# Performance work log

Measured on AMD Instinct MI355X. Metric: run time of the kernel, lower is better.

## Reference

```python
import jax, jax.numpy as jnp
import numpy as np

STEEPNESS = 10.0
EPS = 1e-12

def _l2norm(x):
    return x / jnp.sqrt(jnp.sum(x * x, axis=-1, keepdims=True) + EPS)

def setup_inputs() -> dict:
    key = jax.random.key(0)
    k1, k2, k3 = jax.random.split(key, 3)
    B, D, C = 65536, 512, 1024
    return {
        "query": jax.random.normal(k1, (B, D), dtype=jnp.float32),
        "key_mem": jax.random.normal(k2, (C, D), dtype=jnp.float32),
        "val_mem": jax.random.normal(k3, (C, C), dtype=jnp.float32),
    }

def reference(query, key_mem, val_mem):
    # F.normalize(query_vectors, dim=-1)
    q = _l2norm(query)                      # (B, D)
    # cosine_similarity_multi(q, key_mem, rep='real'):
    # F.linear(F.normalize(a), F.normalize(b)) -> (B, C)
    k = _l2norm(key_mem)                    # (C, D)
    sim = jnp.einsum('bd,cd->bc', q, k)     # (B, C)
    # softabs sharpening: sigmoid(s*(x-0.5)) + sigmoid(s*(-x-0.5))
    s = STEEPNESS
    sharp = jax.nn.sigmoid(s * sim - 0.5 * s) + jax.nn.sigmoid(-s * sim - 0.5 * s)
    # normalize_weightings
    w = sharp / jnp.sum(sharp, axis=1, keepdims=True)
    # weighted value readout
    out = jnp.matmul(w, val_mem)            # (B, C)
    return out
```

## Files before the change

kernel.cpp:

```cpp
#include <hip/hip_runtime.h>
#include <hip/hip_bf16.h>

typedef __attribute__((ext_vector_type(8))) short bf16x8;
typedef __attribute__((ext_vector_type(8))) unsigned short ushort8;
typedef __attribute__((ext_vector_type(4))) float f32x4;
typedef unsigned int u32;

#define D_DIM 512
#define C_DIM 1024

__device__ __forceinline__ unsigned short f2bf(float x) {
  u32 u = __float_as_uint(x);
  u32 r = (u + 0x7fffu + ((u >> 16) & 1u)) >> 16;
  return (unsigned short)r;
}

__device__ __forceinline__ void async16(const void* g, void* l) {
  __builtin_amdgcn_global_load_lds(
      (const __attribute__((address_space(1))) u32*)g,
      (__attribute__((address_space(3))) u32*)l, 16, 0, 0);
}

__device__ __forceinline__ float sharpf(float x) {
  float t = __expf(10.f * x - 5.f);
  return t * __builtin_amdgcn_rcpf(1.f + t) +
         __builtin_amdgcn_rcpf(1.f + t * 22026.4658f);
}

__global__ __launch_bounds__(256) void rownorm_kernel(
    const float* __restrict__ src, unsigned short* __restrict__ dst) {
  int row = blockIdx.x * 4 + (threadIdx.x >> 6);
  int lane = threadIdx.x & 63;
  const float* s = src + (size_t)row * D_DIM + lane * 8;
  float4 v0 = *(const float4*)s;
  float4 v1 = *(const float4*)(s + 4);
  float ss = v0.x * v0.x + v0.y * v0.y + v0.z * v0.z + v0.w * v0.w +
             v1.x * v1.x + v1.y * v1.y + v1.z * v1.z + v1.w * v1.w;
#pragma unroll
  for (int m = 32; m >= 1; m >>= 1) ss += __shfl_xor(ss, m);
  float rinv = rsqrtf(ss + 1e-12f);
  float tv[8] = {v0.x, v0.y, v0.z, v0.w, v1.x, v1.y, v1.z, v1.w};
  ushort8 o;
#pragma unroll
  for (int i = 0; i < 8; ++i) o[i] = f2bf(tv[i] * rinv);
  *(ushort8*)(dst + (size_t)row * D_DIM + lane * 8) = o;
}

__global__ __launch_bounds__(256) void valT_kernel(
    const float* __restrict__ val, unsigned short* __restrict__ vbT) {
  __shared__ float tile[32][33];
  int bx = blockIdx.x & 31;
  int by = blockIdx.x >> 5;
  int t = threadIdx.x;
  int r = t >> 5, c = t & 31;
#pragma unroll
  for (int i = 0; i < 4; ++i)
    tile[r + i * 8][c] = val[(size_t)(by * 32 + r + i * 8) * C_DIM + bx * 32 + c];
  __syncthreads();
#pragma unroll
  for (int i = 0; i < 4; ++i)
    vbT[(size_t)(bx * 32 + r + i * 8) * C_DIM + by * 32 + c] = f2bf(tile[c][r + i * 8]);
}

template <int K, bool SHARP>
__global__ __launch_bounds__(512, 2) void gemm256_kernel(
    const unsigned short* __restrict__ A, const unsigned short* __restrict__ Bm,
    unsigned short* __restrict__ wout, float* __restrict__ rsum,
    float* __restrict__ fout) {
  __shared__ unsigned short smem[65536];
  const int NKT = K / 64;
  const int bid = blockIdx.x;
  const int wg = (bid & 7) * 128 + (bid >> 3);
  const int m0 = (wg >> 2) * 256;
  const int n0 = (wg & 3) * 256;
  const int t = threadIdx.x;
  const int lane = t & 63;
  const int wv = t >> 6;
  const int wr = wv >> 2;
  const int wc = wv & 3;
  const int lo = lane & 15, hi = lane >> 4;
  const int swu = (lo & 7) << 3;

  const int s_ridx = t >> 3;
  const int s_c = (t & 7) * 8;
  auto stage = [&](int T, int k) {
    int r = (s_ridx < 32) ? (k * 32 + s_ridx) : (96 + k * 32 + s_ridx);
    int cl = s_c ^ ((r & 7) << 3);
    size_t go = (size_t)T * 64 + cl;
    int d = (T & 1) * 32768;
    async16(A + (size_t)(m0 + r) * K + go, &smem[d + r * 64 + s_c]);
    async16(Bm + (size_t)(n0 + r) * K + go, &smem[d + 16384 + r * 64 + s_c]);
  };

  f32x4 acc[8][4];
#pragma unroll
  for (int i = 0; i < 8; ++i)
#pragma unroll
    for (int j = 0; j < 4; ++j) acc[i][j] = (f32x4){0.f, 0.f, 0.f, 0.f};

  stage(0, 0); stage(0, 1); stage(0, 2); stage(0, 3);
  stage(1, 0); stage(1, 1); stage(1, 2);

#pragma unroll 1
  for (int T = 0; T < NKT; ++T) {
    if (T == NKT - 1) {
      asm volatile("s_waitcnt vmcnt(0)" ::: "memory");
    } else {
      asm volatile("s_waitcnt vmcnt(6)" ::: "memory");
    }
    __builtin_amdgcn_s_barrier();
    const int d = (T & 1) * 32768;
    bf16x8 bfr[4][2];
    {
      bf16x8 af[2][2];
#pragma unroll
      for (int mi = 0; mi < 2; ++mi)
#pragma unroll
        for (int ks = 0; ks < 2; ++ks) {
          int r = wr * 128 + mi * 16 + lo;
          af[mi][ks] = *(const bf16x8*)&smem[d + r * 64 + ((ks * 32 + hi * 8) ^ swu)];
        }
#pragma unroll
      for (int nf = 0; nf < 4; ++nf)
#pragma unroll
        for (int ks = 0; ks < 2; ++ks) {
          int r = wc * 64 + nf * 16 + lo;
          bfr[nf][ks] =
              *(const bf16x8*)&smem[d + 16384 + r * 64 + ((ks * 32 + hi * 8) ^ swu)];
        }
      if (T + 1 < NKT) stage(T + 1, 3);
      __builtin_amdgcn_s_setprio(1);
#pragma unroll
      for (int mi = 0; mi < 2; ++mi)
#pragma unroll
        for (int nf = 0; nf < 4; ++nf)
#pragma unroll
          for (int ks = 0; ks < 2; ++ks)
            acc[mi][nf] = __builtin_amdgcn_mfma_f32_16x16x32_bf16(
                af[mi][ks], bfr[nf][ks], acc[mi][nf], 0, 0, 0);
      __builtin_amdgcn_s_setprio(0);
    }
#pragma unroll
    for (int p = 1; p < 4; ++p) {
      bf16x8 af[2][2];
#pragma unroll
      for (int mi = 0; mi < 2; ++mi)
#pragma unroll
        for (int ks = 0; ks < 2; ++ks) {
          int r = wr * 128 + (p * 2 + mi) * 16 + lo;
          af[mi][ks] = *(const bf16x8*)&smem[d + r * 64 + ((ks * 32 + hi * 8) ^ swu)];
        }
      __builtin_amdgcn_s_barrier();
      if (T + 2 < NKT) stage(T + 2, p - 1);
      __builtin_amdgcn_s_setprio(1);
#pragma unroll
      for (int mi = 0; mi < 2; ++mi)
#pragma unroll
        for (int nf = 0; nf < 4; ++nf)
#pragma unroll
          for (int ks = 0; ks < 2; ++ks)
            acc[p * 2 + mi][nf] = __builtin_amdgcn_mfma_f32_16x16x32_bf16(
                af[mi][ks], bfr[nf][ks], acc[p * 2 + mi][nf], 0, 0, 0);
      __builtin_amdgcn_s_setprio(0);
    }
  }
  __syncthreads();

  if (SHARP) {
    float rs[8][4];
#pragma unroll
    for (int i = 0; i < 8; ++i)
#pragma unroll
      for (int j = 0; j < 4; ++j) rs[i][j] = 0.f;
    unsigned short* ep = smem;
#pragma unroll
    for (int mf = 0; mf < 8; ++mf)
#pragma unroll
      for (int nf = 0; nf < 4; ++nf)
#pragma unroll
        for (int j = 0; j < 4; ++j) {
          float s = sharpf(acc[mf][nf][j]);
          rs[mf][j] += s;
          int rl = wr * 128 + mf * 16 + (hi << 2) + j;
          int cl = wc * 64 + nf * 16 + lo;
          ep[rl * 256 + cl] = f2bf(s);
        }
#pragma unroll
    for (int mf = 0; mf < 8; ++mf)
#pragma unroll
      for (int j = 0; j < 4; ++j) {
        float v = rs[mf][j];
        v += __shfl_xor(v, 1);
        v += __shfl_xor(v, 2);
        v += __shfl_xor(v, 4);
        v += __shfl_xor(v, 8);
        if (lo == 0)
          atomicAdd(&rsum[m0 + wr * 128 + mf * 16 + (hi << 2) + j], v);
      }
    __syncthreads();
#pragma unroll
    for (int pass = 0; pass < 16; ++pass) {
      int idx = pass * 4096 + t * 8;
      int row = idx >> 8, col = idx & 255;
      *(ushort8*)&wout[(size_t)(m0 + row) * C_DIM + n0 + col] = *(const ushort8*)&ep[idx];
    }
  } else {
    float rinv[8][4];
#pragma unroll
    for (int mf = 0; mf < 8; ++mf)
#pragma unroll
      for (int j = 0; j < 4; ++j)
        rinv[mf][j] =
            __builtin_amdgcn_rcpf(rsum[m0 + wr * 128 + mf * 16 + (hi << 2) + j]);
#pragma unroll
    for (int mf = 0; mf < 8; ++mf)
#pragma unroll
      for (int nf = 0; nf < 4; ++nf)
#pragma unroll
        for (int j = 0; j < 4; ++j)
          fout[(size_t)(m0 + wr * 128 + mf * 16 + (hi << 2) + j) * C_DIM +
               n0 + wc * 64 + nf * 16 + lo] = acc[mf][nf][j] * rinv[mf][j];
  }
}

extern "C" void kernel_launch(void* const* d_in, const int* in_sizes, int n_in,
                              void* d_out, int out_size, void* d_ws, size_t ws_size,
                              hipStream_t stream) {
  const float* query = (const float*)d_in[0];
  const float* key = (const float*)d_in[1];
  const float* val = (const float*)d_in[2];
  float* out = (float*)d_out;
  const int B = in_sizes[0] / D_DIM;

  char* ws = (char*)d_ws;
  unsigned short* kb = (unsigned short*)(ws);
  unsigned short* vbT = (unsigned short*)(ws + (1ull << 20));
  float* rsum = (float*)(ws + 3ull * (1ull << 20));
  unsigned short* qb = (unsigned short*)(ws + 4ull * (1ull << 20));
  unsigned short* wbf = (unsigned short*)(ws + 68ull * (1ull << 20));

  rownorm_kernel<<<dim3(B / 4), dim3(256), 0, stream>>>(query, qb);
  rownorm_kernel<<<dim3(C_DIM / 4), dim3(256), 0, stream>>>(key, kb);
  valT_kernel<<<dim3(1024), dim3(256), 0, stream>>>(val, vbT);
  hipMemsetAsync(rsum, 0, (size_t)B * sizeof(float), stream);

  dim3 grid((B / 256) * (C_DIM / 256));
  gemm256_kernel<D_DIM, true><<<grid, dim3(512), 0, stream>>>(qb, kb, wbf, rsum, nullptr);
  gemm256_kernel<C_DIM, false><<<grid, dim3(512), 0, stream>>>(wbf, vbT, nullptr, rsum, out);
}
```

Before: 359.6 us.

## Replace rsum atomics with per-tile partials, swizzle epilogue LDS, single-rcp sharpen

Global atomicAdd row-sum accumulation and the memset are replaced. Each block first reduces its four column-wave sums in LDS and writes a per-n-tile partial, and a small kernel sums the four partials into a buffer that reuses the qb region. The LDS epilogue store gets an XOR swizzle to reduce bank conflicts, and the sharpen function is rewritten as a single rational expression with one reciprocal. This adds an extra kernel launch and extra barriers. The rational form may overflow for large sim values, since t*t can become inf.

```diff
diff --git a/kernel.cpp b/kernel.cpp
--- a/kernel.cpp
+++ b/kernel.cpp
@@ -8,6 +8,7 @@
 
 #define D_DIM 512
 #define C_DIM 1024
+#define B_DIM 65536
 
 __device__ __forceinline__ unsigned short f2bf(float x) {
   u32 u = __float_as_uint(x);
@@ -23,8 +24,10 @@
 
 __device__ __forceinline__ float sharpf(float x) {
   float t = __expf(10.f * x - 5.f);
-  return t * __builtin_amdgcn_rcpf(1.f + t) +
-         __builtin_amdgcn_rcpf(1.f + t * 22026.4658f);
+  float u = 22026.4658f * t * t;
+  float num = u + 2.f * t + 1.f;
+  float den = u + 22027.4658f * t + 1.f;
+  return num * __builtin_amdgcn_rcpf(den);
 }
 
 __global__ __launch_bounds__(256) void rownorm_kernel(
@@ -60,6 +63,13 @@
 #pragma unroll
   for (int i = 0; i < 4; ++i)
     vbT[(size_t)(bx * 32 + r + i * 8) * C_DIM + by * 32 + c] = f2bf(tile[c][r + i * 8]);
+}
+
+__global__ __launch_bounds__(256) void rsum_reduce_kernel(
+    const float* __restrict__ part, float* __restrict__ rsum) {
+  int i = blockIdx.x * 256 + threadIdx.x;
+  rsum[i] = (part[i] + part[i + B_DIM]) +
+            (part[i + 2 * B_DIM] + part[i + 3 * B_DIM]);
 }
 
 template <int K, bool SHARP>
@@ -182,7 +192,7 @@
           float s = sharpf(acc[mf][nf][j]);
           rs[mf][j] += s;
           int rl = wr * 128 + mf * 16 + (hi << 2) + j;
-          int cl = wc * 64 + nf * 16 + lo;
+          int cl = (wc * 64 + nf * 16 + lo) ^ (((rl >> 2) & 3) << 4);
           ep[rl * 256 + cl] = f2bf(s);
         }
 #pragma unroll
@@ -194,15 +204,30 @@
         v += __shfl_xor(v, 2);
         v += __shfl_xor(v, 4);
         v += __shfl_xor(v, 8);
-        if (lo == 0)
-          atomicAdd(&rsum[m0 + wr * 128 + mf * 16 + (hi << 2) + j], v);
+        rs[mf][j] = v;
       }
     __syncthreads();
 #pragma unroll
     for (int pass = 0; pass < 16; ++pass) {
       int idx = pass * 4096 + t * 8;
       int row = idx >> 8, col = idx & 255;
-      *(ushort8*)&wout[(size_t)(m0 + row) * C_DIM + n0 + col] = *(const ushort8*)&ep[idx];
+      int phys = row * 256 + (col ^ (((row >> 2) & 3) << 4));
+      *(ushort8*)&wout[(size_t)(m0 + row) * C_DIM + n0 + col] =
+          *(const ushort8*)&ep[phys];
+    }
+    __syncthreads();
+    float* rbuf = (float*)smem;
+    if (lo == 0) {
+#pragma unroll
+      for (int mf = 0; mf < 8; ++mf)
+#pragma unroll
+        for (int j = 0; j < 4; ++j)
+          rbuf[wc * 256 + wr * 128 + mf * 16 + (hi << 2) + j] = rs[mf][j];
+    }
+    __syncthreads();
+    if (t < 256) {
+      float v = (rbuf[t] + rbuf[256 + t]) + (rbuf[512 + t] + rbuf[768 + t]);
+      rsum[(size_t)(wg & 3) * B_DIM + m0 + t] = v;
     }
   } else {
     float rinv[8][4];
@@ -235,16 +260,17 @@
   char* ws = (char*)d_ws;
   unsigned short* kb = (unsigned short*)(ws);
   unsigned short* vbT = (unsigned short*)(ws + (1ull << 20));
-  float* rsum = (float*)(ws + 3ull * (1ull << 20));
+  float* rsum_part = (float*)(ws + 3ull * (1ull << 20));
   unsigned short* qb = (unsigned short*)(ws + 4ull * (1ull << 20));
+  float* rsum = (float*)qb;
   unsigned short* wbf = (unsigned short*)(ws + 68ull * (1ull << 20));
 
   rownorm_kernel<<<dim3(B / 4), dim3(256), 0, stream>>>(query, qb);
   rownorm_kernel<<<dim3(C_DIM / 4), dim3(256), 0, stream>>>(key, kb);
   valT_kernel<<<dim3(1024), dim3(256), 0, stream>>>(val, vbT);
-  hipMemsetAsync(rsum, 0, (size_t)B * sizeof(float), stream);
 
   dim3 grid((B / 256) * (C_DIM / 256));
-  gemm256_kernel<D_DIM, true><<<grid, dim3(512), 0, stream>>>(qb, kb, wbf, rsum, nullptr);
+  gemm256_kernel<D_DIM, true><<<grid, dim3(512), 0, stream>>>(qb, kb, wbf, rsum_part, nullptr);
+  rsum_reduce_kernel<<<dim3(B / 256), dim3(256), 0, stream>>>(rsum_part, rsum);
   gemm256_kernel<C_DIM, false><<<grid, dim3(512), 0, stream>>>(wbf, vbT, nullptr, rsum, out);
 }
```

After: 326.1 us. -9.3%, faster.
